# Optimization experiments

Measured on AMD Instinct MI355X. Metric: run time of the kernel, lower is better.

Reference implementation:

```python
import jax, jax.numpy as jnp
import numpy as np

N = 50_000          # nodes
E = 1_600_000       # edges (avg degree 32)
F_IN = 8            # num_static_node_features
F_OUT = 12          # num_timesteps_in (TGCN hidden)
PERIODS = 6         # num_timesteps_out


def setup_inputs() -> dict:
    key = jax.random.key(0)
    ks = jax.random.split(key, 12)
    def n(k, shape, s=0.2):
        return jax.random.normal(k, shape, jnp.float32) * s
    return {
        "x": jax.random.normal(ks[0], (N, F_IN, PERIODS), jnp.float32),
        "edge_index": jax.random.randint(ks[1], (2, E), 0, N, dtype=jnp.int32),
        "edge_weight": jax.random.uniform(ks[2], (E,), jnp.float32),
        "att": n(ks[3], (PERIODS,), 1.0),
        "Wz": n(ks[4], (F_IN, F_OUT)), "bz": jnp.zeros((F_OUT,), jnp.float32),
        "Wr": n(ks[5], (F_IN, F_OUT)), "br": jnp.zeros((F_OUT,), jnp.float32),
        "Wh": n(ks[6], (F_IN, F_OUT)), "bh": jnp.zeros((F_OUT,), jnp.float32),
        "lzW": n(ks[7], (F_OUT, 2 * F_OUT)), "lzb": jnp.zeros((F_OUT,), jnp.float32),
        "lrW": n(ks[8], (F_OUT, 2 * F_OUT)), "lrb": jnp.zeros((F_OUT,), jnp.float32),
        "lhW": n(ks[9], (F_OUT, 2 * F_OUT)), "lhb": jnp.zeros((F_OUT,), jnp.float32),
        "linW": n(ks[10], (PERIODS, F_OUT)), "linb": jnp.zeros((PERIODS,), jnp.float32),
    }


def _gcn_norm(edge_index, edge_weight):
    # PyG gcn_norm: add self loops (weight 1.0), symmetric D^-1/2 A D^-1/2,
    # degree computed from dst (col) of edge_weight.
    src, dst = edge_index[0], edge_index[1]
    loop = jnp.arange(N, dtype=src.dtype)
    src = jnp.concatenate([src, loop])
    dst = jnp.concatenate([dst, loop])
    ew = jnp.concatenate([edge_weight, jnp.ones((N,), edge_weight.dtype)])
    deg = jax.ops.segment_sum(ew, dst, num_segments=N)
    dinv = jnp.where(deg > 0, 1.0 / jnp.sqrt(deg), 0.0)
    return src, dst, dinv[src] * ew * dinv[dst]


def _gcn_conv(xp, W, b, src, dst, norm):
    h = xp @ W                                  # [N, F_OUT]
    msg = norm[:, None] * h[src]                # gather over edges
    return jax.ops.segment_sum(msg, dst, num_segments=N) + b


def reference(x, edge_index, edge_weight, att, Wz, bz, Wr, br, Wh, bh,
              lzW, lzb, lrW, lrb, lhW, lhb, linW, linb):
    src, dst, norm = _gcn_norm(edge_index, edge_weight)
    H0 = jnp.zeros((N, F_OUT), x.dtype)  # A3TGCN passes H=None each period

    def tgcn_cell(xp):  # xp: [N, F_IN]
        Z = jax.nn.sigmoid(
            jnp.concatenate([_gcn_conv(xp, Wz, bz, src, dst, norm), H0], -1) @ lzW.T + lzb)
        R = jax.nn.sigmoid(
            jnp.concatenate([_gcn_conv(xp, Wr, br, src, dst, norm), H0], -1) @ lrW.T + lrb)
        Ht = jnp.tanh(
            jnp.concatenate([_gcn_conv(xp, Wh, bh, src, dst, norm), H0 * R], -1) @ lhW.T + lhb)
        return Z * H0 + (1.0 - Z) * Ht

    probs = jax.nn.softmax(att)                  # [P]
    Hs = jax.vmap(tgcn_cell, in_axes=2)(x)       # [P, N, F_OUT]
    H = jnp.einsum('p,pnf->nf', probs, Hs)       # attention-weighted sum
    h = jax.nn.relu(H)
    return h @ linW.T + linb                     # [N, PERIODS]
```

## Files before the change

kernel.cpp:

```cpp
#include <hip/hip_runtime.h>
#include <hip/hip_fp16.h>

#define N_NODES 50000
#define N_EDGES 1600000
#define F_IN 8
#define F_OUT 12
#define PERIODS 6
#define FP 48
#define BKT_SH 7
#define BKT_N 128
#define NBKT ((N_NODES + BKT_N - 1) / BKT_N)
#define CHK 4096
#define NCHK ((N_EDGES + CHK - 1) / CHK)
#define SEG_CAP 4736

__global__ void k_zero(unsigned int* __restrict__ cursor) {
    int i = threadIdx.x;
    if (i < NBKT) cursor[i] = 0u;
}

__global__ void __launch_bounds__(512) k_scatter(const int4* __restrict__ src4,
                                                 const int4* __restrict__ dst4,
                                                 const float4* __restrict__ ew4,
                                                 unsigned int* __restrict__ cursor,
                                                 unsigned long long* __restrict__ part) {
    __shared__ unsigned int h[NBKT];
    __shared__ unsigned int gbase[NBKT];
    int tid = threadIdx.x, blk = blockIdx.x;
    for (int k = tid; k < NBKT; k += 512) h[k] = 0u;
    __syncthreads();
    int qbase = blk * (CHK / 4);
    int bv[8]; unsigned int lr[8], lo[8], hiw[8]; bool val[8];
    #pragma unroll
    for (int u = 0; u < 2; u++) {
        int q = qbase + u * 512 + tid;
        bool v = (q < N_EDGES / 4);
        int4 ss = v ? src4[q] : make_int4(0, 0, 0, 0);
        int4 dd = v ? dst4[q] : make_int4(0, 0, 0, 0);
        float4 ww = v ? ew4[q] : make_float4(0.f, 0.f, 0.f, 0.f);
        int s[4] = { ss.x, ss.y, ss.z, ss.w };
        int d[4] = { dd.x, dd.y, dd.z, dd.w };
        float w[4] = { ww.x, ww.y, ww.z, ww.w };
        #pragma unroll
        for (int e = 0; e < 4; e++) {
            int i = u * 4 + e;
            val[i] = v;
            if (v) {
                int b = d[e] >> BKT_SH;
                bv[i] = b;
                lr[i] = atomicAdd(&h[b], 1u);
                lo[i] = ((unsigned int)(d[e] & (BKT_N - 1)) << 24) | (unsigned int)s[e];
                hiw[i] = __float_as_uint(w[e]);
            }
        }
    }
    __syncthreads();
    for (int k = tid; k < NBKT; k += 512) {
        unsigned int c = h[k];
        gbase[k] = c ? atomicAdd(&cursor[k], c) : 0u;
    }
    __syncthreads();
    #pragma unroll
    for (int i = 0; i < 8; i++) {
        if (!val[i]) continue;
        unsigned int off = gbase[bv[i]] + lr[i];
        if (off < SEG_CAP)
            part[(size_t)bv[i] * SEG_CAP + off] =
                ((unsigned long long)hiw[i] << 32) | lo[i];
    }
}

__global__ void __launch_bounds__(512) k_bucket(const unsigned long long* __restrict__ part,
                                                const unsigned int* __restrict__ cursor,
                                                const float* __restrict__ x,
                                                int2* __restrict__ offs2,
                                                float* __restrict__ dinv_g,
                                                uint4* __restrict__ xs,
                                                unsigned int* __restrict__ csr4) {
    __shared__ uint2 stage[SEG_CAP];
    __shared__ unsigned int cnt[BKT_N], rowstart[BKT_N], sc[BKT_N];
    __shared__ float degf[BKT_N], dinv_l[BKT_N];
    int tid = threadIdx.x, k = blockIdx.x;
    unsigned int base = (unsigned int)k * SEG_CAP;
    unsigned int m = cursor[k];
    if (m > SEG_CAP) m = SEG_CAP;
    if (tid < BKT_N) { cnt[tid] = 0u; degf[tid] = 1.0f; }
    __syncthreads();

    for (unsigned int i = tid; i < m; i += 512) {
        unsigned long long p = __builtin_nontemporal_load(&part[base + i]);
        unsigned int lo = (unsigned int)p;
        unsigned int hi = (unsigned int)(p >> 32);
        unsigned int j = (lo >> 24) & (BKT_N - 1);
        unsigned int r = atomicAdd(&cnt[j], 1u);
        atomicAdd(&degf[j], __uint_as_float(hi));
        if (r > 255u) r = 255u;
        stage[i] = make_uint2(lo | (r << 16), hi);
    }
    __syncthreads();

    if (tid < 64) {
        unsigned int a = cnt[tid], b = cnt[tid + 64];
        unsigned int sa = a;
        #pragma unroll
        for (int off = 1; off < 64; off <<= 1) {
            unsigned int tv = __shfl_up(sa, off);
            if ((tid & 63) >= off) sa += tv;
        }
        unsigned int tot = __shfl(sa, 63);
        unsigned int sb = b;
        #pragma unroll
        for (int off = 1; off < 64; off <<= 1) {
            unsigned int tv = __shfl_up(sb, off);
            if ((tid & 63) >= off) sb += tv;
        }
        sc[tid] = sa;
        sc[tid + 64] = sb + tot;
    }
    __syncthreads();

    int n0 = k * BKT_N;
    int nn = N_NODES - n0; if (nn > BKT_N) nn = BKT_N;

    if (tid < BKT_N) {
        unsigned int rs = sc[tid] - cnt[tid];
        rowstart[tid] = rs;
        float dv = rsqrtf(degf[tid]);
        dinv_l[tid] = dv;
        if (tid < nn) {
            dinv_g[n0 + tid] = dv;
            offs2[n0 + tid] = make_int2((int)(base + rs), (int)(base + sc[tid]));
        }
    }
    __syncthreads();

    for (unsigned int i = tid; i < m; i += 512) {
        uint2 vv = stage[i];
        unsigned int j = (vv.x >> 24) & (BKT_N - 1);
        unsigned int r = (vv.x >> 16) & 0xFFu;
        __half hw = __float2half(__uint_as_float(vv.y));
        unsigned int entry = ((unsigned int)__half_as_ushort(hw) << 16) |
                             (vv.x & 0xFFFFu);
        csr4[base + rowstart[j] + r] = entry;
    }

    for (int idx = tid; idx < nn * 6; idx += 512) {
        int j = idx / 6, c = idx % 6;
        float di = dinv_l[j];
        const float4* xr = (const float4*)(x + (size_t)(n0 + j) * FP + c * 8);
        float4 a = xr[0], b = xr[1];
        __half2 h0 = __floats2half2_rn(di * a.x, di * a.y);
        __half2 h1 = __floats2half2_rn(di * a.z, di * a.w);
        __half2 h2 = __floats2half2_rn(di * b.x, di * b.y);
        __half2 h3 = __floats2half2_rn(di * b.z, di * b.w);
        uint4 o;
        o.x = *(unsigned int*)&h0; o.y = *(unsigned int*)&h1;
        o.z = *(unsigned int*)&h2; o.w = *(unsigned int*)&h3;
        xs[(size_t)(n0 + j) * 6 + c] = o;
    }
}

__global__ void __launch_bounds__(256) k_gather(const uint4* __restrict__ xs,
                                                const float* __restrict__ dinv,
                                                const int2* __restrict__ offs2,
                                                const unsigned int* __restrict__ csr4,
                                                uint4* __restrict__ xagg) {
    int t = blockIdx.x * 256 + threadIdx.x;
    if (t >= N_NODES * 24) return;
    int n = t / 24, r = t % 24, c = r >> 2, g = r & 3;
    int2 oe = offs2[n];
    const unsigned int* rowp = csr4 + oe.x;
    int cnt = oe.y - oe.x;
    float a0 = 0.f, a1 = 0.f, a2 = 0.f, a3 = 0.f;
    float a4 = 0.f, a5 = 0.f, a6 = 0.f, a7 = 0.f;
    int kk = 0;
    for (; kk + 16 <= cnt; kk += 16) {
        unsigned int p[4]; uint4 v[4];
        #pragma unroll
        for (int u = 0; u < 4; u++)
            p[u] = __builtin_nontemporal_load(rowp + kk + 4 * u + g);
        #pragma unroll
        for (int u = 0; u < 4; u++)
            v[u] = xs[(size_t)(p[u] & 0xFFFFu) * 6 + c];
        #pragma unroll
        for (int u = 0; u < 4; u++) {
            float w = __half2float(__ushort_as_half((unsigned short)(p[u] >> 16)));
            float2 e0 = __half22float2(*(__half2*)&v[u].x);
            float2 e1 = __half22float2(*(__half2*)&v[u].y);
            float2 e2 = __half22float2(*(__half2*)&v[u].z);
            float2 e3 = __half22float2(*(__half2*)&v[u].w);
            a0 += w * e0.x; a1 += w * e0.y; a2 += w * e1.x; a3 += w * e1.y;
            a4 += w * e2.x; a5 += w * e2.y; a6 += w * e3.x; a7 += w * e3.y;
        }
    }
    for (int j = kk + g; j < cnt; j += 4) {
        unsigned int p = __builtin_nontemporal_load(rowp + j);
        float w = __half2float(__ushort_as_half((unsigned short)(p >> 16)));
        uint4 v = xs[(size_t)(p & 0xFFFFu) * 6 + c];
        float2 e0 = __half22float2(*(__half2*)&v.x);
        float2 e1 = __half22float2(*(__half2*)&v.y);
        float2 e2 = __half22float2(*(__half2*)&v.z);
        float2 e3 = __half22float2(*(__half2*)&v.w);
        a0 += w * e0.x; a1 += w * e0.y; a2 += w * e1.x; a3 += w * e1.y;
        a4 += w * e2.x; a5 += w * e2.y; a6 += w * e3.x; a7 += w * e3.y;
    }
    a0 += __shfl_xor(a0, 1); a1 += __shfl_xor(a1, 1);
    a2 += __shfl_xor(a2, 1); a3 += __shfl_xor(a3, 1);
    a4 += __shfl_xor(a4, 1); a5 += __shfl_xor(a5, 1);
    a6 += __shfl_xor(a6, 1); a7 += __shfl_xor(a7, 1);
    a0 += __shfl_xor(a0, 2); a1 += __shfl_xor(a1, 2);
    a2 += __shfl_xor(a2, 2); a3 += __shfl_xor(a3, 2);
    a4 += __shfl_xor(a4, 2); a5 += __shfl_xor(a5, 2);
    a6 += __shfl_xor(a6, 2); a7 += __shfl_xor(a7, 2);
    if (g == 0) {
        uint4 sf = xs[(size_t)n * 6 + c];
        float2 s0 = __half22float2(*(__half2*)&sf.x);
        float2 s1 = __half22float2(*(__half2*)&sf.y);
        float2 s2 = __half22float2(*(__half2*)&sf.z);
        float2 s3 = __half22float2(*(__half2*)&sf.w);
        a0 += s0.x; a1 += s0.y; a2 += s1.x; a3 += s1.y;
        a4 += s2.x; a5 += s2.y; a6 += s3.x; a7 += s3.y;
        float di = dinv[n];
        __half2 h0 = __floats2half2_rn(di * a0, di * a1);
        __half2 h1 = __floats2half2_rn(di * a2, di * a3);
        __half2 h2 = __floats2half2_rn(di * a4, di * a5);
        __half2 h3 = __floats2half2_rn(di * a6, di * a7);
        uint4 o;
        o.x = *(unsigned int*)&h0; o.y = *(unsigned int*)&h1;
        o.z = *(unsigned int*)&h2; o.w = *(unsigned int*)&h3;
        xagg[(size_t)n * 6 + c] = o;
    }
}

__global__ void k_node(const uint4* __restrict__ xagg, const float* __restrict__ att,
                       const float* __restrict__ Wz, const float* __restrict__ bz,
                       const float* __restrict__ Wh, const float* __restrict__ bh,
                       const float* __restrict__ lzW, const float* __restrict__ lzb,
                       const float* __restrict__ lhW, const float* __restrict__ lhb,
                       const float* __restrict__ linW, const float* __restrict__ linb,
                       float* __restrict__ out) {
    int n = blockIdx.x * blockDim.x + threadIdx.x;
    if (n >= N_NODES) return;

    float a[PERIODS];
    float m = -1e30f;
    #pragma unroll
    for (int p = 0; p < PERIODS; p++) { a[p] = att[p]; m = fmaxf(m, a[p]); }
    float se = 0.f;
    #pragma unroll
    for (int p = 0; p < PERIODS; p++) { a[p] = __expf(a[p] - m); se += a[p]; }
    float inv = 1.f / se;
    #pragma unroll
    for (int p = 0; p < PERIODS; p++) a[p] *= inv;

    float row[FP];
    const uint4* xr = xagg + (size_t)n * 6;
    #pragma unroll
    for (int i = 0; i < 6; i++) {
        uint4 v = xr[i];
        float2 f0 = __half22float2(*(__half2*)&v.x);
        float2 f1 = __half22float2(*(__half2*)&v.y);
        float2 f2 = __half22float2(*(__half2*)&v.z);
        float2 f3 = __half22float2(*(__half2*)&v.w);
        row[8 * i + 0] = f0.x; row[8 * i + 1] = f0.y;
        row[8 * i + 2] = f1.x; row[8 * i + 3] = f1.y;
        row[8 * i + 4] = f2.x; row[8 * i + 5] = f2.y;
        row[8 * i + 6] = f3.x; row[8 * i + 7] = f3.y;
    }

    float H[F_OUT];
    #pragma unroll
    for (int j = 0; j < F_OUT; j++) H[j] = 0.f;

    for (int p = 0; p < PERIODS; p++) {
        float gz[F_OUT], gh[F_OUT];
        #pragma unroll
        for (int j = 0; j < F_OUT; j++) { gz[j] = bz[j]; gh[j] = bh[j]; }
        #pragma unroll
        for (int f = 0; f < F_IN; f++) {
            float xv = row[f * PERIODS + p];
            #pragma unroll
            for (int j = 0; j < F_OUT; j++) {
                gz[j] += xv * Wz[f * F_OUT + j];
                gh[j] += xv * Wh[f * F_OUT + j];
            }
        }
        #pragma unroll
        for (int j = 0; j < F_OUT; j++) {
            float z = lzb[j], t2 = lhb[j];
            #pragma unroll
            for (int kk = 0; kk < F_OUT; kk++) {
                z  += gz[kk] * lzW[j * (2 * F_OUT) + kk];
                t2 += gh[kk] * lhW[j * (2 * F_OUT) + kk];
            }
            float Z = 1.f / (1.f + __expf(-z));
            float e2 = __expf(2.f * t2);
            float th = 1.f - __fdividef(2.f, e2 + 1.f);
            H[j] += a[p] * (1.f - Z) * th;
        }
    }

    float* op = out + (size_t)n * PERIODS;
    #pragma unroll
    for (int q = 0; q < PERIODS; q++) {
        float acc = linb[q];
        #pragma unroll
        for (int j = 0; j < F_OUT; j++)
            acc += fmaxf(H[j], 0.f) * linW[q * F_OUT + j];
        op[q] = acc;
    }
}

extern "C" void kernel_launch(void* const* d_in, const int* in_sizes, int n_in,
                              void* d_out, int out_size, void* d_ws, size_t ws_size,
                              hipStream_t stream) {
    const float* x    = (const float*)d_in[0];
    const int*   ei   = (const int*)d_in[1];
    const float* ew   = (const float*)d_in[2];
    const float* att  = (const float*)d_in[3];
    const float* Wz   = (const float*)d_in[4];
    const float* bz   = (const float*)d_in[5];
    const float* Wh   = (const float*)d_in[8];
    const float* bh   = (const float*)d_in[9];
    const float* lzW  = (const float*)d_in[10];
    const float* lzb  = (const float*)d_in[11];
    const float* lhW  = (const float*)d_in[14];
    const float* lhb  = (const float*)d_in[15];
    const float* linW = (const float*)d_in[16];
    const float* linb = (const float*)d_in[17];
    float* out = (float*)d_out;

    uint4* xs   = (uint4*)d_ws;
    uint4* xagg = xs + (size_t)N_NODES * 6;
    unsigned long long* part = (unsigned long long*)(xagg + (size_t)N_NODES * 6);
    unsigned int* csr4 = (unsigned int*)(part + (size_t)NBKT * SEG_CAP);
    int2*  offs2 = (int2*)(csr4 + (size_t)NBKT * SEG_CAP);
    float* dinv  = (float*)(offs2 + N_NODES);
    unsigned int* cursor = (unsigned int*)(dinv + N_NODES);

    const int* srcp = ei;
    const int* dstp = ei + N_EDGES;

    k_zero<<<1, 512, 0, stream>>>(cursor);
    k_scatter<<<NCHK, 512, 0, stream>>>((const int4*)srcp, (const int4*)dstp,
                                        (const float4*)ew, cursor, part);
    k_bucket<<<NBKT, 512, 0, stream>>>(part, cursor, x, offs2, dinv, xs, csr4);
    k_gather<<<(N_NODES * 24 + 255) / 256, 256, 0, stream>>>(xs, dinv, offs2, csr4, xagg);
    k_node<<<(N_NODES + 255) / 256, 256, 0, stream>>>(xagg, att, Wz, bz, Wh, bh,
                                                      lzW, lzb, lhW, lhb, linW, linb, out);
}
```

Baseline: 208.5 us.

## Fuse edge gather and per-node TGCN/attention compute into one kernel

Merges the gather kernel and the per-node cell kernel into a single kernel. Each block of 192 threads handles 8 nodes: aggregated features stay in shared memory as fp32, and the gate matmuls, activations and output projection are spread across threads with block barriers in between. This removes the fp16 xagg round trip through global memory and one kernel launch, and it makes the node compute run across several threads per node instead of one. The cost is three __syncthreads per block and idle lanes in the later phases (only 12 or 6 of 24 threads per node active). The precision of the aggregated values also changes because they are no longer rounded to fp16.

```diff
diff --git a/kernel.cpp b/kernel.cpp
--- a/kernel.cpp
+++ b/kernel.cpp
@@ -160,14 +160,31 @@
     }
 }
 
-__global__ void __launch_bounds__(256) k_gather(const uint4* __restrict__ xs,
-                                                const float* __restrict__ dinv,
-                                                const int2* __restrict__ offs2,
-                                                const unsigned int* __restrict__ csr4,
-                                                uint4* __restrict__ xagg) {
-    int t = blockIdx.x * 256 + threadIdx.x;
-    if (t >= N_NODES * 24) return;
-    int n = t / 24, r = t % 24, c = r >> 2, g = r & 3;
+__global__ void __launch_bounds__(192) k_gnode(const uint4* __restrict__ xs,
+                                               const float* __restrict__ dinv,
+                                               const int2* __restrict__ offs2,
+                                               const unsigned int* __restrict__ csr4,
+                                               const float* __restrict__ att,
+                                               const float* __restrict__ Wz,
+                                               const float* __restrict__ bz,
+                                               const float* __restrict__ Wh,
+                                               const float* __restrict__ bh,
+                                               const float* __restrict__ lzW,
+                                               const float* __restrict__ lzb,
+                                               const float* __restrict__ lhW,
+                                               const float* __restrict__ lhb,
+                                               const float* __restrict__ linW,
+                                               const float* __restrict__ linb,
+                                               float* __restrict__ out) {
+    __shared__ float row[8][48];
+    __shared__ float gzs[8][72];
+    __shared__ float ghs[8][72];
+    __shared__ float Hl[8][12];
+
+    int tid = threadIdx.x;
+    int L = tid / 24, r = tid % 24, c = r >> 2, g = r & 3;
+    int n = blockIdx.x * 8 + L;
+
     int2 oe = offs2[n];
     const unsigned int* rowp = csr4 + oe.x;
     int cnt = oe.y - oe.x;
@@ -193,8 +210,8 @@
             a4 += w * e2.x; a5 += w * e2.y; a6 += w * e3.x; a7 += w * e3.y;
         }
     }
-    for (int j = kk + g; j < cnt; j += 4) {
-        unsigned int p = __builtin_nontemporal_load(rowp + j);
+    for (int jj = kk + g; jj < cnt; jj += 4) {
+        unsigned int p = __builtin_nontemporal_load(rowp + jj);
         float w = __half2float(__ushort_as_half((unsigned short)(p >> 16)));
         uint4 v = xs[(size_t)(p & 0xFFFFu) * 6 + c];
         float2 e0 = __half22float2(*(__half2*)&v.x);
@@ -218,96 +235,61 @@
         float2 s1 = __half22float2(*(__half2*)&sf.y);
         float2 s2 = __half22float2(*(__half2*)&sf.z);
         float2 s3 = __half22float2(*(__half2*)&sf.w);
-        a0 += s0.x; a1 += s0.y; a2 += s1.x; a3 += s1.y;
-        a4 += s2.x; a5 += s2.y; a6 += s3.x; a7 += s3.y;
         float di = dinv[n];
-        __half2 h0 = __floats2half2_rn(di * a0, di * a1);
-        __half2 h1 = __floats2half2_rn(di * a2, di * a3);
-        __half2 h2 = __floats2half2_rn(di * a4, di * a5);
-        __half2 h3 = __floats2half2_rn(di * a6, di * a7);
-        uint4 o;
-        o.x = *(unsigned int*)&h0; o.y = *(unsigned int*)&h1;
-        o.z = *(unsigned int*)&h2; o.w = *(unsigned int*)&h3;
-        xagg[(size_t)n * 6 + c] = o;
-    }
-}
-
-__global__ void k_node(const uint4* __restrict__ xagg, const float* __restrict__ att,
-                       const float* __restrict__ Wz, const float* __restrict__ bz,
-                       const float* __restrict__ Wh, const float* __restrict__ bh,
-                       const float* __restrict__ lzW, const float* __restrict__ lzb,
-                       const float* __restrict__ lhW, const float* __restrict__ lhb,
-                       const float* __restrict__ linW, const float* __restrict__ linb,
-                       float* __restrict__ out) {
-    int n = blockIdx.x * blockDim.x + threadIdx.x;
-    if (n >= N_NODES) return;
-
-    float a[PERIODS];
-    float m = -1e30f;
-    #pragma unroll
-    for (int p = 0; p < PERIODS; p++) { a[p] = att[p]; m = fmaxf(m, a[p]); }
-    float se = 0.f;
-    #pragma unroll
-    for (int p = 0; p < PERIODS; p++) { a[p] = __expf(a[p] - m); se += a[p]; }
-    float inv = 1.f / se;
-    #pragma unroll
-    for (int p = 0; p < PERIODS; p++) a[p] *= inv;
-
-    float row[FP];
-    const uint4* xr = xagg + (size_t)n * 6;
-    #pragma unroll
-    for (int i = 0; i < 6; i++) {
-        uint4 v = xr[i];
-        float2 f0 = __half22float2(*(__half2*)&v.x);
-        float2 f1 = __half22float2(*(__half2*)&v.y);
-        float2 f2 = __half22float2(*(__half2*)&v.z);
-        float2 f3 = __half22float2(*(__half2*)&v.w);
-        row[8 * i + 0] = f0.x; row[8 * i + 1] = f0.y;
-        row[8 * i + 2] = f1.x; row[8 * i + 3] = f1.y;
-        row[8 * i + 4] = f2.x; row[8 * i + 5] = f2.y;
-        row[8 * i + 6] = f3.x; row[8 * i + 7] = f3.y;
-    }
-
-    float H[F_OUT];
-    #pragma unroll
-    for (int j = 0; j < F_OUT; j++) H[j] = 0.f;
-
-    for (int p = 0; p < PERIODS; p++) {
-        float gz[F_OUT], gh[F_OUT];
-        #pragma unroll
-        for (int j = 0; j < F_OUT; j++) { gz[j] = bz[j]; gh[j] = bh[j]; }
+        row[L][8 * c + 0] = di * (a0 + s0.x); row[L][8 * c + 1] = di * (a1 + s0.y);
+        row[L][8 * c + 2] = di * (a2 + s1.x); row[L][8 * c + 3] = di * (a3 + s1.y);
+        row[L][8 * c + 4] = di * (a4 + s2.x); row[L][8 * c + 5] = di * (a5 + s2.y);
+        row[L][8 * c + 6] = di * (a6 + s3.x); row[L][8 * c + 7] = di * (a7 + s3.y);
+    }
+    __syncthreads();
+
+    for (int it = r; it < 72; it += 24) {
+        int p = it / 12, q = it - p * 12;
+        float gz = bz[q], gh = bh[q];
         #pragma unroll
         for (int f = 0; f < F_IN; f++) {
-            float xv = row[f * PERIODS + p];
-            #pragma unroll
-            for (int j = 0; j < F_OUT; j++) {
-                gz[j] += xv * Wz[f * F_OUT + j];
-                gh[j] += xv * Wh[f * F_OUT + j];
-            }
-        }
-        #pragma unroll
-        for (int j = 0; j < F_OUT; j++) {
+            float xv = row[L][f * 6 + p];
+            gz += xv * Wz[f * F_OUT + q];
+            gh += xv * Wh[f * F_OUT + q];
+        }
+        gzs[L][it] = gz; ghs[L][it] = gh;
+    }
+    __syncthreads();
+
+    if (r < 12) {
+        float a[PERIODS];
+        float mx = -1e30f;
+        #pragma unroll
+        for (int p = 0; p < PERIODS; p++) { a[p] = att[p]; mx = fmaxf(mx, a[p]); }
+        float se = 0.f;
+        #pragma unroll
+        for (int p = 0; p < PERIODS; p++) { a[p] = __expf(a[p] - mx); se += a[p]; }
+        float inv = 1.f / se;
+        int j = r;
+        float hacc = 0.f;
+        #pragma unroll
+        for (int p = 0; p < PERIODS; p++) {
             float z = lzb[j], t2 = lhb[j];
             #pragma unroll
-            for (int kk = 0; kk < F_OUT; kk++) {
-                z  += gz[kk] * lzW[j * (2 * F_OUT) + kk];
-                t2 += gh[kk] * lhW[j * (2 * F_OUT) + kk];
+            for (int q = 0; q < F_OUT; q++) {
+                z  += gzs[L][p * 12 + q] * lzW[j * (2 * F_OUT) + q];
+                t2 += ghs[L][p * 12 + q] * lhW[j * (2 * F_OUT) + q];
             }
             float Z = 1.f / (1.f + __expf(-z));
             float e2 = __expf(2.f * t2);
             float th = 1.f - __fdividef(2.f, e2 + 1.f);
-            H[j] += a[p] * (1.f - Z) * th;
-        }
-    }
-
-    float* op = out + (size_t)n * PERIODS;
-    #pragma unroll
-    for (int q = 0; q < PERIODS; q++) {
-        float acc = linb[q];
+            hacc += (a[p] * inv) * (1.f - Z) * th;
+        }
+        Hl[L][j] = fmaxf(hacc, 0.f);
+    }
+    __syncthreads();
+
+    if (r < PERIODS) {
+        float acc = linb[r];
         #pragma unroll
         for (int j = 0; j < F_OUT; j++)
-            acc += fmaxf(H[j], 0.f) * linW[q * F_OUT + j];
-        op[q] = acc;
+            acc += Hl[L][j] * linW[r * F_OUT + j];
+        out[(size_t)n * PERIODS + r] = acc;
     }
 }
 
@@ -331,8 +313,7 @@
     float* out = (float*)d_out;
 
     uint4* xs   = (uint4*)d_ws;
-    uint4* xagg = xs + (size_t)N_NODES * 6;
-    unsigned long long* part = (unsigned long long*)(xagg + (size_t)N_NODES * 6);
+    unsigned long long* part = (unsigned long long*)(xs + (size_t)N_NODES * 6);
     unsigned int* csr4 = (unsigned int*)(part + (size_t)NBKT * SEG_CAP);
     int2*  offs2 = (int2*)(csr4 + (size_t)NBKT * SEG_CAP);
     float* dinv  = (float*)(offs2 + N_NODES);
@@ -345,7 +326,7 @@
     k_scatter<<<NCHK, 512, 0, stream>>>((const int4*)srcp, (const int4*)dstp,
                                         (const float4*)ew, cursor, part);
     k_bucket<<<NBKT, 512, 0, stream>>>(part, cursor, x, offs2, dinv, xs, csr4);
-    k_gather<<<(N_NODES * 24 + 255) / 256, 256, 0, stream>>>(xs, dinv, offs2, csr4, xagg);
-    k_node<<<(N_NODES + 255) / 256, 256, 0, stream>>>(xagg, att, Wz, bz, Wh, bh,
-                                                      lzW, lzb, lhW, lhb, linW, linb, out);
-}
+    k_gnode<<<N_NODES / 8, 192, 0, stream>>>(xs, dinv, offs2, csr4, att,
+                                             Wz, bz, Wh, bh, lzW, lzb, lhW, lhb,
+                                             linW, linb, out);
+}
```

New measurement: 187.0 us. 10.3% less time.
